# Performance work log

Hardware: AMD Instinct MI355X
Metric: run time of the kernel (lower is better)

## Reference

```python
import jax, jax.numpy as jnp
import numpy as np

N_NODES = 100000
N_EDGES = 1600000
IN_DIM = 256
OUT_DIM = 128


def setup_inputs() -> dict:
    key = jax.random.key(0)
    ks = jax.random.split(key, 8)
    x = jax.random.normal(ks[0], (N_NODES, IN_DIM), dtype=jnp.float32)
    # glorot-ish init scaling
    W = jax.random.normal(ks[1], (IN_DIM, OUT_DIM), dtype=jnp.float32) * (6.0 / (IN_DIM + OUT_DIM)) ** 0.5
    fsW = jax.random.normal(ks[2], (IN_DIM, OUT_DIM), dtype=jnp.float32) * (6.0 / (IN_DIM + OUT_DIM)) ** 0.5
    f_weights = jax.random.normal(ks[3], (2 * OUT_DIM, 1), dtype=jnp.float32) * (6.0 / (2 * OUT_DIM + 1)) ** 0.5
    f_bias = jnp.zeros((1,), dtype=jnp.float32)
    # degrees in [1, 64], strictly positive so pow(deg, -p) is finite
    dia_adj = jax.random.uniform(ks[4], (N_NODES,), dtype=jnp.float32) * 63.0 + 1.0
    row = jax.random.randint(ks[5], (N_EDGES,), 0, N_NODES, dtype=jnp.int32)
    col = jax.random.randint(ks[6], (N_EDGES,), 0, N_NODES, dtype=jnp.int32)
    return {"x": x, "W": W, "fsW": fsW, "f_weights": f_weights,
            "f_bias": f_bias, "dia_adj": dia_adj, "row": row, "col": col}


def reference(x, W, fsW, f_weights, f_bias, dia_adj, row, col):
    # pre_sup = x @ weights_, fpre_sup = x @ fs_weights  (dropout=0, dense inputs)
    pre_sup = x @ W                 # [N, out]
    fpre_sup = x @ fsW              # [N, out]
    d = W.shape[1]
    # concat([vi, vj]) @ f_weights == vi @ f_weights[:d] + vj @ f_weights[d:]
    wi, wj = f_weights[:d], f_weights[d:]
    score = jax.nn.sigmoid(fpre_sup[row] @ wi + fpre_sup[col] @ wj + f_bias)  # [E, 1]
    # degree-power normalization: (deg_i * deg_j) ** (-sigmoid_score)
    deg_vivj = (dia_adj[row] * dia_adj[col])[:, None]                         # [E, 1]
    vals = jnp.power(deg_vivj, -score)[:, 0]                                  # [E]
    # sparse matmul: out[r] += vals_e * pre_sup[c] for each edge e=(r,c)
    msg = vals[:, None] * pre_sup[col]                                        # [E, out]
    out = jax.ops.segment_sum(msg, row, num_segments=x.shape[0])              # [N, out]
    return jax.nn.relu(out)
```

## Files before the change

kernel.cpp:

```cpp
#include <hip/hip_runtime.h>

#define N_NODES 100000
#define N_EDGES 1600000
#define IN_DIM 256
#define OUT_DIM 128
#define BROWS 100
#define NBK 1000
#define PBLK 128
#define EPB 12500

typedef __attribute__((ext_vector_type(4))) float f32x4;
typedef __attribute__((ext_vector_type(8))) short s16x8;

__device__ inline unsigned short f2bf(float f) {
    union { float f; unsigned int u; } a; a.f = f;
    unsigned int r = a.u + 0x7fffu + ((a.u >> 16) & 1u);
    return (unsigned short)(r >> 16);
}
__device__ inline float bf2f(unsigned short h) {
    union { unsigned int u; float f; } a; a.u = ((unsigned int)h) << 16;
    return a.f;
}
__device__ inline void gload16(const void* g, void* l) {
    __builtin_amdgcn_global_load_lds(
        (const __attribute__((address_space(1))) void*)g,
        (__attribute__((address_space(3))) void*)l, 16, 0, 0);
}

__global__ __launch_bounds__(256) void kprep(
        const float* __restrict__ fsW, const float* __restrict__ fw,
        const float* __restrict__ W, const int* __restrict__ row,
        float* __restrict__ u, float* __restrict__ v,
        unsigned short* __restrict__ wt, int* __restrict__ hist_t) {
    __shared__ int h[NBK];
    __shared__ float wi[128], wj[128];
    const int t = threadIdx.x, blk = blockIdx.x;
    if (blk < PBLK) {
        wt[blk * 256 + t] = f2bf(W[(size_t)t * 128 + blk]);
        for (int b = t; b < NBK; b += 256) h[b] = 0;
        __syncthreads();
        const int e0 = blk * EPB;
        for (int i = t; i < EPB; i += 256)
            atomicAdd(&h[row[e0 + i] / BROWS], 1);
        __syncthreads();
        for (int b = t; b < NBK; b += 256)
            hist_t[b * PBLK + blk] = h[b];
    } else {
        if (t < 128) wi[t] = fw[t]; else wj[t - 128] = fw[t];
        __syncthreads();
        const float* rowp = fsW + (size_t)t * OUT_DIM;
        float su = 0.f, sv = 0.f;
        for (int d = 0; d < 128; d += 4) {
            float4 a = *(const float4*)(rowp + d);
            su += a.x * wi[d] + a.y * wi[d + 1] + a.z * wi[d + 2] + a.w * wi[d + 3];
            sv += a.x * wj[d] + a.y * wj[d + 1] + a.z * wj[d + 2] + a.w * wj[d + 3];
        }
        u[t] = su; v[t] = sv;
    }
}

__global__ __launch_bounds__(1024) void kbscan(const int* __restrict__ hist_t,
                                               int* __restrict__ bpre) {
    __shared__ int s[1024];
    const int t = threadIdx.x;
    int v = 0;
    if (t < NBK) {
        const int4* hp = (const int4*)(hist_t + t * PBLK);
#pragma unroll 4
        for (int k = 0; k < PBLK / 4; ++k) {
            int4 a = hp[k];
            v += a.x + a.y + a.z + a.w;
        }
    }
    s[t] = v;
    __syncthreads();
    for (int off = 1; off < 1024; off <<= 1) {
        int nv = (t >= off) ? s[t - off] : 0;
        __syncthreads();
        s[t] += nv;
        __syncthreads();
    }
    if (t < NBK) bpre[t] = s[t] - v;
    if (t == 1023) bpre[NBK] = s[1023];
}

__global__ __launch_bounds__(128) void koff(const int* __restrict__ hist_t,
                                            const int* __restrict__ bpre,
                                            int* __restrict__ off) {
    const int b = blockIdx.x, t = threadIdx.x;
    const int lane = t & 63, w = t >> 6;
    int v = hist_t[b * PBLK + t];
    int s = v;
#pragma unroll
    for (int o = 1; o < 64; o <<= 1) { int tt = __shfl_up(s, o); if (lane >= o) s += tt; }
    __shared__ int ws2[2];
    if (lane == 63) ws2[w] = s;
    __syncthreads();
    int base = (w == 1) ? ws2[0] : 0;
    off[b * PBLK + t] = bpre[b] + base + (s - v);
}

__global__ __launch_bounds__(256) void gpart(
        const float* __restrict__ x, const unsigned short* __restrict__ wt,
        const float* __restrict__ u, const float* __restrict__ v,
        unsigned short* __restrict__ psb, float* __restrict__ si, float* __restrict__ sj,
        const int* __restrict__ row, const int* __restrict__ col,
        const int* __restrict__ off, unsigned int* __restrict__ part) {
    __shared__ char ldsraw[16640];

    const int t = threadIdx.x;

    if (blockIdx.x < PBLK) {
        int* cur = (int*)ldsraw;
        const int blk = blockIdx.x;
        for (int b = t; b < NBK; b += 256) cur[b] = off[b * PBLK + blk];
        __syncthreads();
        const int e0 = blk * EPB;
        for (int i = t; i < EPB; i += 256) {
            int r = row[e0 + i], c = col[e0 + i];
            int b = r / BROWS;
            int rl = r - b * BROWS;
            int pos = atomicAdd(&cur[b], 1);
            part[pos] = ((unsigned)rl << 17) | (unsigned)c;
        }
        return;
    }

    const int wave = t >> 6, lane = t & 63;
    const int l15 = lane & 15, lhi = lane >> 4;
    const int rw = t >> 2, quad = t & 3;
    const int brow = (blockIdx.x - PBLK) * 64;
    const int gnode = brow + rw;
    const bool valid = gnode < N_NODES;

    f32x4 acc[4][2];
#pragma unroll
    for (int mi = 0; mi < 4; ++mi)
#pragma unroll
        for (int ni = 0; ni < 2; ++ni) acc[mi][ni] = (f32x4){0.f, 0.f, 0.f, 0.f};
    float su = 0.f, sv = 0.f;

#pragma unroll
    for (int ph = 0; ph < 4; ++ph) {
#pragma unroll
        for (int i = 0; i < 4; ++i) {
            int lo = i * 4096 + t * 16;
            int q  = lo ^ (((lo >> 8) & 7) << 4);
            int grow = brow + (q >> 8);
            if (grow >= N_NODES) grow = N_NODES - 1;
            gload16((const char*)x + (size_t)grow * 1024 + ph * 256 + (q & 255),
                    ldsraw + lo);
        }
        __syncthreads();

        {
            const unsigned short* wb0 = wt + (size_t)(wave * 32 + l15) * IN_DIM + ph * 64 + lhi * 8;
            s16x8 bfr[2][2];
#pragma unroll
            for (int ks = 0; ks < 2; ++ks) {
                bfr[ks][0] = *(const s16x8*)(wb0 + ks * 32);
                bfr[ks][1] = *(const s16x8*)(wb0 + (size_t)16 * IN_DIM + ks * 32);
            }
#pragma unroll
            for (int ks = 0; ks < 2; ++ks) {
                s16x8 afr[4];
#pragma unroll
                for (int mi = 0; mi < 4; ++mi) {
                    const int r = mi * 16 + l15;
                    const int sw = (r & 7) << 4;
                    const int b0 = r * 256 + ks * 128 + lhi * 32;
                    float4 f0 = *(const float4*)(ldsraw + (b0 ^ sw));
                    float4 f1 = *(const float4*)(ldsraw + ((b0 + 16) ^ sw));
                    union { unsigned int w[4]; s16x8 s; } cv;
                    asm("v_cvt_pk_bf16_f32 %0, %1, %2" : "=v"(cv.w[0]) : "v"(f0.x), "v"(f0.y));
                    asm("v_cvt_pk_bf16_f32 %0, %1, %2" : "=v"(cv.w[1]) : "v"(f0.z), "v"(f0.w));
                    asm("v_cvt_pk_bf16_f32 %0, %1, %2" : "=v"(cv.w[2]) : "v"(f1.x), "v"(f1.y));
                    asm("v_cvt_pk_bf16_f32 %0, %1, %2" : "=v"(cv.w[3]) : "v"(f1.z), "v"(f1.w));
                    afr[mi] = cv.s;
                }
#pragma unroll
                for (int mi = 0; mi < 4; ++mi)
#pragma unroll
                    for (int ni = 0; ni < 2; ++ni)
                        acc[mi][ni] = __builtin_amdgcn_mfma_f32_16x16x32_bf16(
                            afr[mi], bfr[ks][ni], acc[mi][ni], 0, 0, 0);
            }
        }

        {
            const float* up = u + ph * 64 + quad * 16;
            const float* vp = v + ph * 64 + quad * 16;
            const int rb_ = rw * 256 + quad * 64;
            const int sw = (rw & 7) << 4;
#pragma unroll
            for (int c = 0; c < 4; ++c) {
                float4 a = *(const float4*)(ldsraw + ((rb_ + c * 16) ^ sw));
                float4 uu = ((const float4*)up)[c];
                float4 vv = ((const float4*)vp)[c];
                su = fmaf(a.x, uu.x, su); su = fmaf(a.y, uu.y, su);
                su = fmaf(a.z, uu.z, su); su = fmaf(a.w, uu.w, su);
                sv = fmaf(a.x, vv.x, sv); sv = fmaf(a.y, vv.y, sv);
                sv = fmaf(a.z, vv.z, sv); sv = fmaf(a.w, vv.w, sv);
            }
        }
        __syncthreads();
    }

    su += __shfl_xor(su, 1); su += __shfl_xor(su, 2);
    sv += __shfl_xor(sv, 1); sv += __shfl_xor(sv, 2);
    if (quad == 0 && valid) { si[gnode] = su; sj[gnode] = sv; }

    unsigned short* cl = (unsigned short*)ldsraw;
#pragma unroll
    for (int mi = 0; mi < 4; ++mi)
#pragma unroll
        for (int ni = 0; ni < 2; ++ni) {
            const int colb = wave * 32 + ni * 16 + l15;
#pragma unroll
            for (int j = 0; j < 4; ++j)
                cl[(mi * 16 + lhi * 4 + j) * 128 + colb] = f2bf(acc[mi][ni][j]);
        }
    __syncthreads();
    {
        const int rl = t >> 2;
        const int cb = (t & 3) * 32;
        if (brow + rl < N_NODES) {
            const uint4* src = (const uint4*)&cl[rl * 128 + cb];
            uint4* dst = (uint4*)&psb[(size_t)(brow + rl) * OUT_DIM + cb];
            dst[0] = src[0]; dst[1] = src[1]; dst[2] = src[2]; dst[3] = src[3];
        }
    }
}

__global__ __launch_bounds__(256) void kpart2(const unsigned int* __restrict__ part,
                                              const int* __restrict__ bpre,
                                              const float* __restrict__ si,
                                              const float* __restrict__ sj,
                                              const float* __restrict__ dia,
                                              const float* __restrict__ fb,
                                              int2* __restrict__ epack,
                                              int* __restrict__ offs,
                                              int* __restrict__ deg) {
    __shared__ int cnt[BROWS];
    __shared__ int cur[BROWS];
    __shared__ float sil[BROWS], dial[BROWS];
    __shared__ int wtot[4];
    const int b = blockIdx.x, t = threadIdx.x;
    const int rbase = b * BROWS;
    if (t < BROWS) {
        cnt[t] = 0;
        sil[t] = si[rbase + t];
        dial[t] = dia[rbase + t];
    }
    __syncthreads();
    const int bstart = bpre[b], bend = bpre[b + 1];
    for (int e = bstart + t; e < bend; e += 256)
        atomicAdd(&cnt[part[e] >> 17], 1);
    __syncthreads();
    {
        int vv = (t < BROWS) ? cnt[t] : 0;
        int lane = t & 63, w = t >> 6;
        int s = vv;
#pragma unroll
        for (int o = 1; o < 64; o <<= 1) { int tt = __shfl_up(s, o); if (lane >= o) s += tt; }
        if (lane == 63) wtot[w] = s;
        __syncthreads();
        int base = 0;
        for (int k = 0; k < w; ++k) base += wtot[k];
        int excl = base + s - vv;
        if (t < BROWS) {
            cur[t] = bstart + excl;
            offs[rbase + t] = bstart + excl;
            deg[rbase + t] = vv;
        }
    }
    __syncthreads();
    const float fbv = fb[0];
    for (int e = bstart + t; e < bend; e += 256) {
        unsigned pk = part[e];
        int rl = (int)(pk >> 17);
        int c = (int)(pk & 0x1FFFFu);
        float tval = sil[rl] + sj[c] + fbv;
        float sg = 1.f / (1.f + expf(-tval));
        float l2 = log2f(dial[rl] * dia[c]);
        float val = exp2f(-sg * l2);
        int pos = atomicAdd(&cur[rl], 1);
        epack[pos] = make_int2(c, __float_as_int(val));
    }
}

__global__ __launch_bounds__(256) void kgather(
        const int* __restrict__ offs, const int* __restrict__ deg,
        const int2* __restrict__ epack,
        const unsigned short* __restrict__ psb, float* __restrict__ out) {
    int lane = threadIdx.x & 31;
    int node = blockIdx.x * 8 + (threadIdx.x >> 5);
    if (node >= N_NODES) return;
    int start = offs[node], d = deg[node];
    const int2* ep = epack + start;
    float a0 = 0.f, a1 = 0.f, a2 = 0.f, a3 = 0.f;
    int k = 0;
    for (; k + 8 <= d; k += 8) {
        int2 e0 = ep[k],     e1 = ep[k + 1], e2 = ep[k + 2], e3 = ep[k + 3];
        int2 e4 = ep[k + 4], e5 = ep[k + 5], e6 = ep[k + 6], e7 = ep[k + 7];
        ushort4 p0 = *(const ushort4*)&psb[(size_t)e0.x * OUT_DIM + lane * 4];
        ushort4 p1 = *(const ushort4*)&psb[(size_t)e1.x * OUT_DIM + lane * 4];
        ushort4 p2 = *(const ushort4*)&psb[(size_t)e2.x * OUT_DIM + lane * 4];
        ushort4 p3 = *(const ushort4*)&psb[(size_t)e3.x * OUT_DIM + lane * 4];
        ushort4 p4 = *(const ushort4*)&psb[(size_t)e4.x * OUT_DIM + lane * 4];
        ushort4 p5 = *(const ushort4*)&psb[(size_t)e5.x * OUT_DIM + lane * 4];
        ushort4 p6 = *(const ushort4*)&psb[(size_t)e6.x * OUT_DIM + lane * 4];
        ushort4 p7 = *(const ushort4*)&psb[(size_t)e7.x * OUT_DIM + lane * 4];
        float v0 = __int_as_float(e0.y), v1 = __int_as_float(e1.y);
        float v2 = __int_as_float(e2.y), v3 = __int_as_float(e3.y);
        float v4 = __int_as_float(e4.y), v5 = __int_as_float(e5.y);
        float v6 = __int_as_float(e6.y), v7 = __int_as_float(e7.y);
        a0 = fmaf(v0, bf2f(p0.x), a0); a1 = fmaf(v0, bf2f(p0.y), a1);
        a2 = fmaf(v0, bf2f(p0.z), a2); a3 = fmaf(v0, bf2f(p0.w), a3);
        a0 = fmaf(v1, bf2f(p1.x), a0); a1 = fmaf(v1, bf2f(p1.y), a1);
        a2 = fmaf(v1, bf2f(p1.z), a2); a3 = fmaf(v1, bf2f(p1.w), a3);
        a0 = fmaf(v2, bf2f(p2.x), a0); a1 = fmaf(v2, bf2f(p2.y), a1);
        a2 = fmaf(v2, bf2f(p2.z), a2); a3 = fmaf(v2, bf2f(p2.w), a3);
        a0 = fmaf(v3, bf2f(p3.x), a0); a1 = fmaf(v3, bf2f(p3.y), a1);
        a2 = fmaf(v3, bf2f(p3.z), a2); a3 = fmaf(v3, bf2f(p3.w), a3);
        a0 = fmaf(v4, bf2f(p4.x), a0); a1 = fmaf(v4, bf2f(p4.y), a1);
        a2 = fmaf(v4, bf2f(p4.z), a2); a3 = fmaf(v4, bf2f(p4.w), a3);
        a0 = fmaf(v5, bf2f(p5.x), a0); a1 = fmaf(v5, bf2f(p5.y), a1);
        a2 = fmaf(v5, bf2f(p5.z), a2); a3 = fmaf(v5, bf2f(p5.w), a3);
        a0 = fmaf(v6, bf2f(p6.x), a0); a1 = fmaf(v6, bf2f(p6.y), a1);
        a2 = fmaf(v6, bf2f(p6.z), a2); a3 = fmaf(v6, bf2f(p6.w), a3);
        a0 = fmaf(v7, bf2f(p7.x), a0); a1 = fmaf(v7, bf2f(p7.y), a1);
        a2 = fmaf(v7, bf2f(p7.z), a2); a3 = fmaf(v7, bf2f(p7.w), a3);
    }
    for (; k < d; ++k) {
        int2 e0 = ep[k];
        float v0 = __int_as_float(e0.y);
        ushort4 p0 = *(const ushort4*)&psb[(size_t)e0.x * OUT_DIM + lane * 4];
        a0 = fmaf(v0, bf2f(p0.x), a0);
        a1 = fmaf(v0, bf2f(p0.y), a1);
        a2 = fmaf(v0, bf2f(p0.z), a2);
        a3 = fmaf(v0, bf2f(p0.w), a3);
    }
    float4 o;
    o.x = fmaxf(a0, 0.f); o.y = fmaxf(a1, 0.f);
    o.z = fmaxf(a2, 0.f); o.w = fmaxf(a3, 0.f);
    *(float4*)&out[(size_t)node * OUT_DIM + lane * 4] = o;
}

extern "C" void kernel_launch(void* const* d_in, const int* in_sizes, int n_in,
                              void* d_out, int out_size, void* d_ws, size_t ws_size,
                              hipStream_t stream) {
    const float* x   = (const float*)d_in[0];
    const float* W   = (const float*)d_in[1];
    const float* fsW = (const float*)d_in[2];
    const float* fw  = (const float*)d_in[3];
    const float* fb  = (const float*)d_in[4];
    const float* dia = (const float*)d_in[5];
    const int*   row = (const int*)d_in[6];
    const int*   col = (const int*)d_in[7];
    float* out = (float*)d_out;

    char* p = (char*)d_ws;
    auto alloc = [&](size_t bytes) -> char* {
        char* r = p; p += (bytes + 255) & ~(size_t)255; return r;
    };
    float* u      = (float*)alloc(256 * 4);
    float* v      = (float*)alloc(256 * 4);
    unsigned short* wtb = (unsigned short*)alloc((size_t)128 * 256 * 2);
    float* si     = (float*)alloc((size_t)N_NODES * 4);
    float* sj     = (float*)alloc((size_t)N_NODES * 4);
    int*   deg    = (int*)alloc((size_t)N_NODES * 4);
    int*   offs   = (int*)alloc((size_t)N_NODES * 4);
    unsigned short* psb = (unsigned short*)alloc((size_t)N_NODES * OUT_DIM * 2);
    int*   hist_t = (int*)alloc((size_t)NBK * PBLK * 4);
    int*   bpre   = (int*)alloc((size_t)(NBK + 1) * 4);
    int*   off    = (int*)alloc((size_t)NBK * PBLK * 4);
    unsigned int* part = (unsigned int*)alloc((size_t)N_EDGES * 4);
    int2*  epack  = (int2*)alloc((size_t)N_EDGES * 8);

    kprep<<<PBLK + 1, 256, 0, stream>>>(fsW, fw, W, row, u, v, wtb, hist_t);
    kbscan<<<1, 1024, 0, stream>>>(hist_t, bpre);
    koff<<<NBK, PBLK, 0, stream>>>(hist_t, bpre, off);
    gpart<<<PBLK + (N_NODES + 63) / 64, 256, 0, stream>>>(
        x, wtb, u, v, psb, si, sj, row, col, off, part);
    kpart2<<<NBK, 256, 0, stream>>>(part, bpre, si, sj, dia, fb, epack, offs, deg);
    kgather<<<N_NODES / 8, 256, 0, stream>>>(offs, deg, epack, psb, out);
}
```

Before: 174.4 us.

## Double-buffer x tile loads in GEMM phase to overlap global loads with MFMA

The fused projection kernel now keeps two LDS buffers for the x tiles. It issues the async global-to-LDS loads for the next K-phase before computing on the current one, and uses explicit vmcnt waits and barriers instead of full __syncthreads. This aims to hide global load latency behind MFMA and the score dot products. In exchange LDS use per block roughly doubles, which may lower occupancy, and correctness depends on the hand-placed waitcnt counts.

Result: no change. 175.2 us (+0.5%).

```diff
diff --git a/kernel.cpp b/kernel.cpp
--- a/kernel.cpp
+++ b/kernel.cpp
@@ -106,7 +106,7 @@
         unsigned short* __restrict__ psb, float* __restrict__ si, float* __restrict__ sj,
         const int* __restrict__ row, const int* __restrict__ col,
         const int* __restrict__ off, unsigned int* __restrict__ part) {
-    __shared__ char ldsraw[16640];
+    __shared__ char ldsraw[32896];
 
     const int t = threadIdx.x;
 
@@ -140,18 +140,32 @@
         for (int ni = 0; ni < 2; ++ni) acc[mi][ni] = (f32x4){0.f, 0.f, 0.f, 0.f};
     float su = 0.f, sv = 0.f;
 
+#define STAGE(PH, BUFOFS)                                                        \
+    {                                                                            \
+        _Pragma("unroll")                                                        \
+        for (int i_ = 0; i_ < 4; ++i_) {                                         \
+            int lo_ = i_ * 4096 + t * 16;                                        \
+            int q_ = lo_ ^ (((lo_ >> 8) & 7) << 4);                              \
+            int grow_ = brow + (q_ >> 8);                                        \
+            if (grow_ >= N_NODES) grow_ = N_NODES - 1;                           \
+            gload16((const char*)x + (size_t)grow_ * 1024 + (PH) * 256 + (q_ & 255), \
+                    ldsraw + (BUFOFS) + lo_);                                    \
+        }                                                                        \
+    }
+
+    STAGE(0, 0);
+
 #pragma unroll
     for (int ph = 0; ph < 4; ++ph) {
-#pragma unroll
-        for (int i = 0; i < 4; ++i) {
-            int lo = i * 4096 + t * 16;
-            int q  = lo ^ (((lo >> 8) & 7) << 4);
-            int grow = brow + (q >> 8);
-            if (grow >= N_NODES) grow = N_NODES - 1;
-            gload16((const char*)x + (size_t)grow * 1024 + ph * 256 + (q & 255),
-                    ldsraw + lo);
-        }
-        __syncthreads();
+        const int bufofs = (ph & 1) * 16448;
+        if (ph < 3) {
+            STAGE(ph + 1, ((ph + 1) & 1) * 16448);
+            asm volatile("s_waitcnt vmcnt(4)" ::: "memory");
+        } else {
+            asm volatile("s_waitcnt vmcnt(0)" ::: "memory");
+        }
+        __builtin_amdgcn_s_barrier();
+        __builtin_amdgcn_sched_barrier(0);
 
         {
             const unsigned short* wb0 = wt + (size_t)(wave * 32 + l15) * IN_DIM + ph * 64 + lhi * 8;
@@ -169,8 +183,8 @@
                     const int r = mi * 16 + l15;
                     const int sw = (r & 7) << 4;
                     const int b0 = r * 256 + ks * 128 + lhi * 32;
-                    float4 f0 = *(const float4*)(ldsraw + (b0 ^ sw));
-                    float4 f1 = *(const float4*)(ldsraw + ((b0 + 16) ^ sw));
+                    float4 f0 = *(const float4*)(ldsraw + bufofs + (b0 ^ sw));
+                    float4 f1 = *(const float4*)(ldsraw + bufofs + ((b0 + 16) ^ sw));
                     union { unsigned int w[4]; s16x8 s; } cv;
                     asm("v_cvt_pk_bf16_f32 %0, %1, %2" : "=v"(cv.w[0]) : "v"(f0.x), "v"(f0.y));
                     asm("v_cvt_pk_bf16_f32 %0, %1, %2" : "=v"(cv.w[1]) : "v"(f0.z), "v"(f0.w));
@@ -194,7 +208,7 @@
             const int sw = (rw & 7) << 4;
 #pragma unroll
             for (int c = 0; c < 4; ++c) {
-                float4 a = *(const float4*)(ldsraw + ((rb_ + c * 16) ^ sw));
+                float4 a = *(const float4*)(ldsraw + bufofs + ((rb_ + c * 16) ^ sw));
                 float4 uu = ((const float4*)up)[c];
                 float4 vv = ((const float4*)vp)[c];
                 su = fmaf(a.x, uu.x, su); su = fmaf(a.y, uu.y, su);
@@ -203,8 +217,10 @@
                 sv = fmaf(a.z, vv.z, sv); sv = fmaf(a.w, vv.w, sv);
             }
         }
-        __syncthreads();
-    }
+        asm volatile("s_waitcnt lgkmcnt(0)" ::: "memory");
+        __builtin_amdgcn_s_barrier();
+    }
+#undef STAGE
 
     su += __shfl_xor(su, 1); su += __shfl_xor(su, 2);
     sv += __shfl_xor(sv, 1); sv += __shfl_xor(sv, 2);
```
